# Kernel optimization log

Measured on AMD Instinct MI355X. Metric: run time of the kernel, lower is better.

Reference implementation:

```python
import jax, jax.numpy as jnp
import numpy as np

B, S, D = 8, 2048, 1024      # batch, seq (tokens), in/out token dim
E = 2 * D                    # expansion dim (expansion_factor=2)
SDIM = 128                   # attention feature dim s
SQRT_S = float(np.sqrt(SDIM))
EPS_LN = 1e-5                # ScaleNorm eps


def setup_inputs() -> dict:
    key = jax.random.key(0)
    ks = jax.random.split(key, 8)
    return {
        "x": jax.random.normal(ks[0], (B, S, D), jnp.float32),
        "pos_enc": jax.random.normal(ks[1], (S, SDIM), jnp.float32),
        "ln_g": jnp.ones((1,), jnp.float32),                                   # ScaleNorm scalar gain
        "uv_w": jax.random.normal(ks[2], (2 * E + SDIM, D), jnp.float32) / np.sqrt(D),  # fused uv proj (xavier-ish)
        "gamma": jax.random.uniform(ks[3], (2, SDIM), jnp.float32),            # q/k affine scale
        "beta": jax.random.uniform(ks[4], (2, SDIM), jnp.float32),             # q/k affine shift
        "o_w": jax.random.normal(ks[5], (D, E), jnp.float32) / np.sqrt(E),     # output proj
        "res_scale": jnp.ones((D,), jnp.float32),                              # ChannelWiseScale
    }


def reference(x, pos_enc, ln_g, uv_w, gamma, beta, o_w, res_scale):
    # ScaleNorm: x / clamp(||x|| * d^-0.5, eps) * g
    norm = jnp.linalg.norm(x, axis=-1, keepdims=True) * (D ** -0.5)
    xn = x / jnp.maximum(norm, EPS_LN) * ln_g
    # fused uv projection + SiLU
    uv = jax.nn.silu(xn @ uv_w.T)                      # [B,S,2E+s]
    u = uv[..., :E]                                    # gate
    v = uv[..., E:2 * E]                               # values
    base = uv[..., 2 * E:]                             # shared q/k base [B,S,s]
    qk_base = base[..., None, :] * gamma + beta        # [B,S,2,s]
    q = qk_base[..., 0, :] + pos_enc                   # add positional enc [B,S,s]
    k = qk_base[..., 1, :] + pos_enc
    # squared-ReLU attention kernel
    kernel = jnp.square(jax.nn.relu(jnp.einsum('bqs,bks->bqk', q, k) / SQRT_S))
    out = (u * jnp.einsum('bqk,bke->bqe', kernel, v)) @ o_w.T  # [B,S,D]
    # channel-wise scaled residual (in_dims == out_dims -> shortcut)
    return x * res_scale + out
```

## Files before the change

### kernel.cpp

```cpp
#include <hip/hip_runtime.h>
#include <stdint.h>

#define B_   8
#define S_   2048
#define D_   1024
#define E_   2048
#define SD_  128
#define M_   (B_ * S_)
#define NUV  (2 * E_ + SD_)

typedef __attribute__((ext_vector_type(8))) short short8;
typedef __attribute__((ext_vector_type(4))) float floatx4;

typedef __attribute__((address_space(1))) void as1_void;
typedef __attribute__((address_space(3))) void as3_void;

__device__ __forceinline__ ushort f2bf(float f) {
    uint32_t u = __float_as_uint(f);
    uint32_t r = (u + 0x7fffu + ((u >> 16) & 1u)) >> 16;
    return (ushort)r;
}
__device__ __forceinline__ float bf2f(ushort h) {
    return __uint_as_float(((uint32_t)h) << 16);
}
__device__ __forceinline__ float silu(float z) {
    return z * __builtin_amdgcn_rcpf(1.0f + __expf(-z));
}

__device__ __forceinline__ void gld_lds16(const ushort* g, ushort* l) {
    __builtin_amdgcn_global_load_lds((const as1_void*)g, (as3_void*)l, 16, 0, 0);
}

__device__ __forceinline__ void tile_swizzle(int& mt, int& nt) {
    const int gx  = gridDim.x;
    const int lin = blockIdx.y * gx + blockIdx.x;
    const int band = lin / (gx * 8);
    const int r    = lin - band * gx * 8;
    mt = band * 8 + (r & 7);
    nt = r >> 3;
}

__device__ __forceinline__ void gemm_core(
    const ushort* __restrict__ A, const ushort* __restrict__ B,
    int lda, int ldb, int K, int m0, int n0,
    ushort* ldsA, ushort* ldsB, floatx4 acc[4][4])
{
    const int t    = threadIdx.x;
    const int lane = t & 63;
    const int l15  = lane & 15;
    const int quad = lane >> 4;
    const int wave = t >> 6;
    const int wm   = (wave >> 1) * 64;
    const int wn   = (wave & 1) * 64;
    const int key  = l15 & 7;

    const ushort* gA[4]; const ushort* gB[4];
    ushort* lA[4]; ushort* lB[4];
    #pragma unroll
    for (int i = 0; i < 4; ++i) {
        const int c   = t + i * 256;
        const int row = c >> 3;
        const int kcl = c & 7;
        const int gkc = kcl ^ (row & 7);
        gA[i] = A + (size_t)(m0 + row) * lda + gkc * 8;
        gB[i] = B + (size_t)(n0 + row) * ldb + gkc * 8;
        lA[i] = ldsA + c * 8;
        lB[i] = ldsB + c * 8;
    }

    for (int kk = 0; kk < K; kk += 64) {
        __syncthreads();
        #pragma unroll
        for (int i = 0; i < 4; ++i) gld_lds16(gA[i] + kk, lA[i]);
        #pragma unroll
        for (int i = 0; i < 4; ++i) gld_lds16(gB[i] + kk, lB[i]);
        __syncthreads();

        #pragma unroll
        for (int s = 0; s < 2; ++s) {
            const int koff = ((s * 4 + quad) ^ key) * 8;
            short8 af[4], bfr[4];
            #pragma unroll
            for (int mi = 0; mi < 4; ++mi)
                af[mi] = *(const short8*)(ldsA + (wm + mi * 16 + l15) * 64 + koff);
            #pragma unroll
            for (int ni = 0; ni < 4; ++ni)
                bfr[ni] = *(const short8*)(ldsB + (wn + ni * 16 + l15) * 64 + koff);
            #pragma unroll
            for (int mi = 0; mi < 4; ++mi)
                #pragma unroll
                for (int ni = 0; ni < 4; ++ni)
                    acc[mi][ni] = __builtin_amdgcn_mfma_f32_16x16x32_bf16(
                        af[mi], bfr[ni], acc[mi][ni], 0, 0, 0);
        }
    }
}

#define EPI_INDICES \
    const int t = threadIdx.x; \
    const int lane = t & 63, l15 = lane & 15, quad = lane >> 4; \
    const int wave = t >> 6, wm = (wave >> 1) * 64, wn = (wave & 1) * 64; \
    (void)t;

#define ZERO_ACC \
    floatx4 acc[4][4]; \
    _Pragma("unroll") \
    for (int i = 0; i < 4; ++i) \
        _Pragma("unroll") \
        for (int j = 0; j < 4; ++j) \
            _Pragma("unroll") \
            for (int r = 0; r < 4; ++r) acc[i][j][r] = 0.0f;

__global__ __launch_bounds__(256) void k_cvt(const float* __restrict__ src,
                                             ushort* __restrict__ dst, int n4) {
    int i = blockIdx.x * 256 + threadIdx.x;
    if (i < n4) {
        float4 v = ((const float4*)src)[i];
        ushort4 o;
        o.x = f2bf(v.x); o.y = f2bf(v.y); o.z = f2bf(v.z); o.w = f2bf(v.w);
        ((ushort4*)dst)[i] = o;
    }
}

__global__ __launch_bounds__(256) void k_rmsnorm(const float* __restrict__ x,
                                                 const float* __restrict__ ln_g,
                                                 ushort* __restrict__ xnb) {
    const int m = blockIdx.x;
    const int t = threadIdx.x;
    float4 v = ((const float4*)(x + (size_t)m * D_))[t];
    float ss = v.x * v.x + v.y * v.y + v.z * v.z + v.w * v.w;
    #pragma unroll
    for (int off = 32; off > 0; off >>= 1) ss += __shfl_down(ss, off, 64);
    __shared__ float red[4];
    if ((t & 63) == 0) red[t >> 6] = ss;
    __syncthreads();
    float tot = red[0] + red[1] + red[2] + red[3];
    float rms = sqrtf(tot * (1.0f / (float)D_));
    float scale = ln_g[0] / fmaxf(rms, 1e-5f);
    ushort4 o;
    o.x = f2bf(v.x * scale); o.y = f2bf(v.y * scale);
    o.z = f2bf(v.z * scale); o.w = f2bf(v.w * scale);
    ((ushort4*)(xnb + (size_t)m * D_))[t] = o;
}

__global__ __launch_bounds__(256) void k_transpose_v(const ushort* __restrict__ v,
                                                     ushort* __restrict__ vT) {
    const int b = blockIdx.z;
    const int e0 = blockIdx.x * 64, s0 = blockIdx.y * 64;
    __shared__ ushort tile[64][65];
    const ushort* vb = v + (size_t)b * S_ * E_;
    ushort* vTb = vT + (size_t)b * E_ * S_;
    const int t = threadIdx.x;
    #pragma unroll
    for (int i = 0; i < 16; ++i) {
        int idx = t + i * 256, r = idx >> 6, c = idx & 63;
        tile[r][c] = vb[(size_t)(s0 + r) * E_ + e0 + c];
    }
    __syncthreads();
    #pragma unroll
    for (int i = 0; i < 16; ++i) {
        int idx = t + i * 256, r = idx >> 6, c = idx & 63;
        vTb[(size_t)(e0 + r) * S_ + s0 + c] = tile[c][r];
    }
}

__global__ __launch_bounds__(256) void k_gemm1(
    const ushort* __restrict__ xnb, const ushort* __restrict__ uvwb,
    const float* __restrict__ gamma, const float* __restrict__ beta,
    const float* __restrict__ pos,
    ushort* __restrict__ u, ushort* __restrict__ v,
    ushort* __restrict__ qb, ushort* __restrict__ kb)
{
    __shared__ __align__(16) ushort ldsA[128 * 64];
    __shared__ __align__(16) ushort ldsB[128 * 64];
    ZERO_ACC
    int mt, nt;
    tile_swizzle(mt, nt);
    const int m0 = mt * 128;
    const int n0 = nt * 128;
    gemm_core(xnb, uvwb, D_, D_, D_, m0, n0, ldsA, ldsB, acc);
    EPI_INDICES

    if (nt < 32) {
        ushort* dst = (nt < 16) ? u : v;
        const int nbase = (nt < 16) ? n0 : (n0 - E_);
        #pragma unroll
        for (int mi = 0; mi < 4; ++mi)
            #pragma unroll
            for (int ni = 0; ni < 4; ++ni) {
                const int col = nbase + wn + ni * 16 + l15;
                #pragma unroll
                for (int r = 0; r < 4; ++r) {
                    const int row = m0 + wm + mi * 16 + quad * 4 + r;
                    dst[(size_t)row * E_ + col] = f2bf(silu(acc[mi][ni][r]));
                }
            }
    } else {
        #pragma unroll
        for (int mi = 0; mi < 4; ++mi)
            #pragma unroll
            for (int ni = 0; ni < 4; ++ni) {
                const int sd = wn + ni * 16 + l15;
                const float g0 = gamma[sd], g1 = gamma[SD_ + sd];
                const float be0 = beta[sd], be1 = beta[SD_ + sd];
                #pragma unroll
                for (int r = 0; r < 4; ++r) {
                    const int row = m0 + wm + mi * 16 + quad * 4 + r;
                    const int srow = row & (S_ - 1);
                    float s = silu(acc[mi][ni][r]);
                    const float p = pos[(size_t)srow * SD_ + sd];
                    qb[(size_t)row * SD_ + sd] = f2bf(s * g0 + be0 + p);
                    kb[(size_t)row * SD_ + sd] = f2bf(s * g1 + be1 + p);
                }
            }
    }
}

__global__ __launch_bounds__(256) void k_scores(
    const ushort* __restrict__ qb, const ushort* __restrict__ kb,
    ushort* __restrict__ kern, int b_off)
{
    __shared__ __align__(16) ushort ldsA[128 * 64];
    __shared__ __align__(16) ushort ldsB[128 * 64];
    ZERO_ACC
    const int bz = blockIdx.z;
    const int b  = b_off + bz;
    int mt, nt;
    tile_swizzle(mt, nt);
    const int m0 = mt * 128;
    const int n0 = nt * 128;
    gemm_core(qb + (size_t)b * S_ * SD_, kb + (size_t)b * S_ * SD_,
              SD_, SD_, SD_, m0, n0, ldsA, ldsB, acc);
    EPI_INDICES
    ushort* ko = kern + (size_t)bz * S_ * S_;
    const float inv = 0.08838834764831845f;
    #pragma unroll
    for (int mi = 0; mi < 4; ++mi)
        #pragma unroll
        for (int ni = 0; ni < 4; ++ni) {
            const int col = n0 + wn + ni * 16 + l15;
            #pragma unroll
            for (int r = 0; r < 4; ++r) {
                const int row = m0 + wm + mi * 16 + quad * 4 + r;
                float s = fmaxf(acc[mi][ni][r] * inv, 0.0f);
                ko[(size_t)row * S_ + col] = f2bf(s * s);
            }
        }
}

__global__ __launch_bounds__(256) void k_kv(
    const ushort* __restrict__ kern, const ushort* __restrict__ vT,
    const ushort* __restrict__ u, ushort* __restrict__ kvu, int b_off)
{
    __shared__ __align__(16) ushort ldsA[128 * 64];
    __shared__ __align__(16) ushort ldsB[128 * 64];
    ZERO_ACC
    const int bz = blockIdx.z;
    const int b  = b_off + bz;
    int mt, nt;
    tile_swizzle(mt, nt);
    const int m0 = mt * 128;
    const int n0 = nt * 128;
    gemm_core(kern + (size_t)bz * S_ * S_, vT + (size_t)b * E_ * S_,
              S_, S_, S_, m0, n0, ldsA, ldsB, acc);
    EPI_INDICES
    #pragma unroll
    for (int mi = 0; mi < 4; ++mi)
        #pragma unroll
        for (int ni = 0; ni < 4; ++ni) {
            const int col = n0 + wn + ni * 16 + l15;
            #pragma unroll
            for (int r = 0; r < 4; ++r) {
                const int row = m0 + wm + mi * 16 + quad * 4 + r;
                const size_t gi = (size_t)(b * S_ + row) * E_ + col;
                float uval = bf2f(u[gi]);
                kvu[gi] = f2bf(uval * acc[mi][ni][r]);
            }
        }
}

__global__ __launch_bounds__(256) void k_out(
    const ushort* __restrict__ kvu, const ushort* __restrict__ owb,
    const float* __restrict__ x, const float* __restrict__ res_scale,
    float* __restrict__ out)
{
    __shared__ __align__(16) ushort ldsA[128 * 64];
    __shared__ __align__(16) ushort ldsB[128 * 64];
    ZERO_ACC
    int mt, nt;
    tile_swizzle(mt, nt);
    const int m0 = mt * 128;
    const int n0 = nt * 128;
    gemm_core(kvu, owb, E_, E_, E_, m0, n0, ldsA, ldsB, acc);
    EPI_INDICES
    #pragma unroll
    for (int mi = 0; mi < 4; ++mi)
        #pragma unroll
        for (int ni = 0; ni < 4; ++ni) {
            const int col = n0 + wn + ni * 16 + l15;
            const float rs = res_scale[col];
            #pragma unroll
            for (int r = 0; r < 4; ++r) {
                const int row = m0 + wm + mi * 16 + quad * 4 + r;
                const size_t gi = (size_t)row * D_ + col;
                out[gi] = x[gi] * rs + acc[mi][ni][r];
            }
        }
}

extern "C" void kernel_launch(void* const* d_in, const int* in_sizes, int n_in,
                              void* d_out, int out_size, void* d_ws, size_t ws_size,
                              hipStream_t stream)
{
    const float* x         = (const float*)d_in[0];
    const float* pos       = (const float*)d_in[1];
    const float* ln_g      = (const float*)d_in[2];
    const float* uv_w      = (const float*)d_in[3];
    const float* gamma     = (const float*)d_in[4];
    const float* beta      = (const float*)d_in[5];
    const float* o_w       = (const float*)d_in[6];
    const float* res_scale = (const float*)d_in[7];
    float* out = (float*)d_out;

    char* p = (char*)d_ws;
    ushort* region0 = (ushort*)p; p += (size_t)M_ * D_ * 2;
    ushort* uvwb    = (ushort*)p; p += (size_t)NUV * D_ * 2;
    ushort* owb     = (ushort*)p; p += (size_t)D_ * E_ * 2;
    ushort* u       = (ushort*)p; p += (size_t)M_ * E_ * 2;
    ushort* region1 = (ushort*)p; p += (size_t)M_ * E_ * 2;
    ushort* vT      = (ushort*)p; p += (size_t)M_ * E_ * 2;
    ushort* qb      = (ushort*)p; p += (size_t)M_ * SD_ * 2;
    ushort* kb      = (ushort*)p; p += (size_t)M_ * SD_ * 2;

    ushort* xnb  = region0;
    ushort* kern = region0;
    ushort* v    = region1;
    ushort* kvu  = region1;

    k_cvt<<<(NUV * D_ / 4 + 255) / 256, 256, 0, stream>>>(uv_w, uvwb, NUV * D_ / 4);
    k_cvt<<<(D_ * E_ / 4 + 255) / 256, 256, 0, stream>>>(o_w, owb, D_ * E_ / 4);
    k_rmsnorm<<<M_, 256, 0, stream>>>(x, ln_g, xnb);
    k_gemm1<<<dim3(NUV / 128, M_ / 128), 256, 0, stream>>>(xnb, uvwb, gamma, beta, pos, u, v, qb, kb);
    k_transpose_v<<<dim3(E_ / 64, S_ / 64, B_), 256, 0, stream>>>(v, vT);
    for (int g = 0; g < 2; ++g) {
        k_scores<<<dim3(S_ / 128, S_ / 128, 4), 256, 0, stream>>>(qb, kb, kern, g * 4);
        k_kv<<<dim3(E_ / 128, S_ / 128, 4), 256, 0, stream>>>(kern, vT, u, kvu, g * 4);
    }
    k_out<<<dim3(D_ / 128, M_ / 128), 256, 0, stream>>>(kvu, owb, x, res_scale, out);
}
```

Measured before the change: 633.1 us.

## Fuse V transpose into gemm1 epilogue and register-prefetch GEMM tiles

```diff
diff --git a/kernel.cpp b/kernel.cpp
--- a/kernel.cpp
+++ b/kernel.cpp
@@ -12,9 +12,6 @@
 typedef __attribute__((ext_vector_type(8))) short short8;
 typedef __attribute__((ext_vector_type(4))) float floatx4;
 
-typedef __attribute__((address_space(1))) void as1_void;
-typedef __attribute__((address_space(3))) void as3_void;
-
 __device__ __forceinline__ ushort f2bf(float f) {
     uint32_t u = __float_as_uint(f);
     uint32_t r = (u + 0x7fffu + ((u >> 16) & 1u)) >> 16;
@@ -25,10 +22,6 @@
 }
 __device__ __forceinline__ float silu(float z) {
     return z * __builtin_amdgcn_rcpf(1.0f + __expf(-z));
-}
-
-__device__ __forceinline__ void gld_lds16(const ushort* g, ushort* l) {
-    __builtin_amdgcn_global_load_lds((const as1_void*)g, (as3_void*)l, 16, 0, 0);
 }
 
 __device__ __forceinline__ void tile_swizzle(int& mt, int& nt) {
@@ -60,21 +53,33 @@
     for (int i = 0; i < 4; ++i) {
         const int c   = t + i * 256;
         const int row = c >> 3;
-        const int kcl = c & 7;
-        const int gkc = kcl ^ (row & 7);
-        gA[i] = A + (size_t)(m0 + row) * lda + gkc * 8;
-        gB[i] = B + (size_t)(n0 + row) * ldb + gkc * 8;
+        const int gkc = ((c & 7) ^ (row & 7)) * 8;
+        gA[i] = A + (size_t)(m0 + row) * lda + gkc;
+        gB[i] = B + (size_t)(n0 + row) * ldb + gkc;
         lA[i] = ldsA + c * 8;
         lB[i] = ldsB + c * 8;
     }
 
+    short8 rA[4], rB[4];
+    #pragma unroll
+    for (int i = 0; i < 4; ++i) rA[i] = *(const short8*)gA[i];
+    #pragma unroll
+    for (int i = 0; i < 4; ++i) rB[i] = *(const short8*)gB[i];
+
     for (int kk = 0; kk < K; kk += 64) {
         __syncthreads();
         #pragma unroll
-        for (int i = 0; i < 4; ++i) gld_lds16(gA[i] + kk, lA[i]);
-        #pragma unroll
-        for (int i = 0; i < 4; ++i) gld_lds16(gB[i] + kk, lB[i]);
+        for (int i = 0; i < 4; ++i) *(short8*)lA[i] = rA[i];
+        #pragma unroll
+        for (int i = 0; i < 4; ++i) *(short8*)lB[i] = rB[i];
         __syncthreads();
+
+        if (kk + 64 < K) {
+            #pragma unroll
+            for (int i = 0; i < 4; ++i) rA[i] = *(const short8*)(gA[i] + kk + 64);
+            #pragma unroll
+            for (int i = 0; i < 4; ++i) rB[i] = *(const short8*)(gB[i] + kk + 64);
+        }
 
         #pragma unroll
         for (int s = 0; s < 2; ++s) {
@@ -143,36 +148,16 @@
     ((ushort4*)(xnb + (size_t)m * D_))[t] = o;
 }
 
-__global__ __launch_bounds__(256) void k_transpose_v(const ushort* __restrict__ v,
-                                                     ushort* __restrict__ vT) {
-    const int b = blockIdx.z;
-    const int e0 = blockIdx.x * 64, s0 = blockIdx.y * 64;
-    __shared__ ushort tile[64][65];
-    const ushort* vb = v + (size_t)b * S_ * E_;
-    ushort* vTb = vT + (size_t)b * E_ * S_;
-    const int t = threadIdx.x;
-    #pragma unroll
-    for (int i = 0; i < 16; ++i) {
-        int idx = t + i * 256, r = idx >> 6, c = idx & 63;
-        tile[r][c] = vb[(size_t)(s0 + r) * E_ + e0 + c];
-    }
-    __syncthreads();
-    #pragma unroll
-    for (int i = 0; i < 16; ++i) {
-        int idx = t + i * 256, r = idx >> 6, c = idx & 63;
-        vTb[(size_t)(e0 + r) * S_ + s0 + c] = tile[c][r];
-    }
-}
-
 __global__ __launch_bounds__(256) void k_gemm1(
     const ushort* __restrict__ xnb, const ushort* __restrict__ uvwb,
     const float* __restrict__ gamma, const float* __restrict__ beta,
     const float* __restrict__ pos,
-    ushort* __restrict__ u, ushort* __restrict__ v,
+    ushort* __restrict__ u, ushort* __restrict__ vT,
     ushort* __restrict__ qb, ushort* __restrict__ kb)
 {
-    __shared__ __align__(16) ushort ldsA[128 * 64];
-    __shared__ __align__(16) ushort ldsB[128 * 64];
+    __shared__ __align__(16) ushort lds[17408];
+    ushort* ldsA = lds;
+    ushort* ldsB = lds + 8192;
     ZERO_ACC
     int mt, nt;
     tile_swizzle(mt, nt);
@@ -181,20 +166,46 @@
     gemm_core(xnb, uvwb, D_, D_, D_, m0, n0, ldsA, ldsB, acc);
     EPI_INDICES
 
-    if (nt < 32) {
-        ushort* dst = (nt < 16) ? u : v;
-        const int nbase = (nt < 16) ? n0 : (n0 - E_);
+    if (nt < 16) {
         #pragma unroll
         for (int mi = 0; mi < 4; ++mi)
             #pragma unroll
             for (int ni = 0; ni < 4; ++ni) {
-                const int col = nbase + wn + ni * 16 + l15;
+                const int col = n0 + wn + ni * 16 + l15;
                 #pragma unroll
                 for (int r = 0; r < 4; ++r) {
                     const int row = m0 + wm + mi * 16 + quad * 4 + r;
-                    dst[(size_t)row * E_ + col] = f2bf(silu(acc[mi][ni][r]));
+                    u[(size_t)row * E_ + col] = f2bf(silu(acc[mi][ni][r]));
                 }
             }
+    } else if (nt < 32) {
+        const int b   = m0 >> 11;
+        const int s0  = m0 & (S_ - 1);
+        const int ec0 = n0 - E_;
+        __syncthreads();
+        #pragma unroll
+        for (int mi = 0; mi < 4; ++mi)
+            #pragma unroll
+            for (int ni = 0; ni < 4; ++ni) {
+                const int col = wn + ni * 16 + l15;
+                const int row = wm + mi * 16 + quad * 4;
+                #pragma unroll
+                for (int r = 0; r < 4; r += 2) {
+                    ushort2 pr;
+                    pr.x = f2bf(silu(acc[mi][ni][r]));
+                    pr.y = f2bf(silu(acc[mi][ni][r + 1]));
+                    *(ushort2*)&lds[col * 136 + row + r] = pr;
+                }
+            }
+        __syncthreads();
+        ushort* vTb = vT + ((size_t)b * E_ + ec0) * S_ + s0;
+        #pragma unroll
+        for (int i = 0; i < 8; ++i) {
+            const int lin = i * 256 + t;
+            const int e  = lin >> 4;
+            const int sb = (lin & 15) * 8;
+            *(short8*)(vTb + (size_t)e * S_ + sb) = *(const short8*)&lds[e * 136 + sb];
+        }
     } else {
         #pragma unroll
         for (int mi = 0; mi < 4; ++mi)
@@ -327,21 +338,18 @@
     ushort* uvwb    = (ushort*)p; p += (size_t)NUV * D_ * 2;
     ushort* owb     = (ushort*)p; p += (size_t)D_ * E_ * 2;
     ushort* u       = (ushort*)p; p += (size_t)M_ * E_ * 2;
-    ushort* region1 = (ushort*)p; p += (size_t)M_ * E_ * 2;
+    ushort* kvu     = (ushort*)p; p += (size_t)M_ * E_ * 2;
     ushort* vT      = (ushort*)p; p += (size_t)M_ * E_ * 2;
     ushort* qb      = (ushort*)p; p += (size_t)M_ * SD_ * 2;
     ushort* kb      = (ushort*)p; p += (size_t)M_ * SD_ * 2;
 
     ushort* xnb  = region0;
     ushort* kern = region0;
-    ushort* v    = region1;
-    ushort* kvu  = region1;
 
     k_cvt<<<(NUV * D_ / 4 + 255) / 256, 256, 0, stream>>>(uv_w, uvwb, NUV * D_ / 4);
     k_cvt<<<(D_ * E_ / 4 + 255) / 256, 256, 0, stream>>>(o_w, owb, D_ * E_ / 4);
     k_rmsnorm<<<M_, 256, 0, stream>>>(x, ln_g, xnb);
-    k_gemm1<<<dim3(NUV / 128, M_ / 128), 256, 0, stream>>>(xnb, uvwb, gamma, beta, pos, u, v, qb, kb);
-    k_transpose_v<<<dim3(E_ / 64, S_ / 64, B_), 256, 0, stream>>>(v, vT);
+    k_gemm1<<<dim3(NUV / 128, M_ / 128), 256, 0, stream>>>(xnb, uvwb, gamma, beta, pos, u, vT, qb, kb);
     for (int g = 0; g < 2; ++g) {
         k_scores<<<dim3(S_ / 128, S_ / 128, 4), 256, 0, stream>>>(qb, kb, kern, g * 4);
         k_kv<<<dim3(E_ / 128, S_ / 128, 4), 256, 0, stream>>>(kern, vT, u, kvu, g * 4);
```

Measured after the change: 648.5 us. 1.02x slower.
